# Kernel tuning notes

Hardware: AMD Instinct MI355X
Metric: run time of the kernel (lower is better)

## Reference

```python
import jax, jax.numpy as jnp
import numpy as np
import math

NUM_LAYERS_HALF = 2   # num_layers // 2
NUM_HEADS = 12
DIM = 768
FFN_DIM = 3072
VOCAB = 50257
BLOCK = 2048
LN_EPS = 1e-5


def _sinusoidal_pe(max_len, dim):
    pos = np.arange(max_len, dtype=np.float32)[:, None]
    div = np.exp(np.arange(0, dim, 2, dtype=np.float32) * (-math.log(10000.0) / dim))
    pe = np.zeros((max_len, dim), dtype=np.float32)
    pe[:, 0::2] = np.sin(pos * div)
    pe[:, 1::2] = np.cos(pos * div)
    return jnp.asarray(pe)[None]  # [1, max_len, dim]


def setup_inputs() -> dict:
    key = jax.random.key(0)
    ks = jax.random.split(key, 16)
    L, D, F = NUM_LAYERS_HALF, DIM, FFN_DIM
    s = 0.02
    return {
        "idx": jax.random.randint(ks[0], (1, 2048), 0, VOCAB),
        "token_emb": jax.random.normal(ks[1], (VOCAB, D), jnp.float32) * s,
        "pe": _sinusoidal_pe(BLOCK, D),
        "qkv_w": jax.random.normal(ks[2], (L, D, 3 * D), jnp.float32) * s,
        "qkv_b": jnp.zeros((L, 3 * D), jnp.float32),
        "out_w": jax.random.normal(ks[3], (L, D, D), jnp.float32) * s,
        "out_b": jnp.zeros((L, D), jnp.float32),
        "ln1_s": jnp.ones((L, D), jnp.float32),
        "ln1_b": jnp.zeros((L, D), jnp.float32),
        "ln2_s": jnp.ones((L, D), jnp.float32),
        "ln2_b": jnp.zeros((L, D), jnp.float32),
        "w1": jax.random.normal(ks[4], (L, D, F), jnp.float32) * s,
        "b1": jnp.zeros((L, F), jnp.float32),
        "w2": jax.random.normal(ks[5], (L, F, D), jnp.float32) * s,
        "b2": jnp.zeros((L, D), jnp.float32),
    }


def _layer_norm(x, scale, bias):
    m = jnp.mean(x, axis=-1, keepdims=True)
    v = jnp.mean(jnp.square(x - m), axis=-1, keepdims=True)
    return (x - m) * jax.lax.rsqrt(v + LN_EPS) * scale + bias


def _forward(idx, token_emb, pe, qkv_w, qkv_b, out_w, out_b,
             ln1_s, ln1_b, ln2_s, ln2_b, w1, b1, w2, b2):
    B, S = idx.shape
    D, H = DIM, NUM_HEADS
    hd = D // H
    x = token_emb[idx] + pe[:, :S]                     # [B,S,D]
    causal = jnp.tril(jnp.ones((S, S), dtype=bool))    # [S,S]

    def block(x, p):
        qw, qb, ow, ob, l1s, l1b, l2s, l2b, fw1, fb1, fw2, fb2 = p
        h = _layer_norm(x, l1s, l1b)
        qkv = (h @ qw + qb).reshape(B, S, 3, H, hd)
        q, k, v = jnp.moveaxis(qkv, 2, 0)              # each [B,S,H,hd]
        q = q.transpose(0, 2, 1, 3)                    # [B,H,S,hd]
        k = k.transpose(0, 2, 1, 3)
        v = v.transpose(0, 2, 1, 3)
        scores = jnp.einsum('bhqd,bhkd->bhqk', q, k) / math.sqrt(hd)
        scores = jnp.where(causal, scores, -1e9)
        attn = jax.nn.softmax(scores, axis=-1)
        o = jnp.einsum('bhqk,bhkd->bhqd', attn, v)
        o = o.transpose(0, 2, 1, 3).reshape(B, S, D)
        x = x + (o @ ow + ob)
        h2 = _layer_norm(x, l2s, l2b)
        ff = jax.nn.gelu(h2 @ fw1 + fb1, approximate=False) @ fw2 + fb2
        return x + ff, None

    params = (qkv_w, qkv_b, out_w, out_b, ln1_s, ln1_b, ln2_s, ln2_b, w1, b1, w2, b2)
    x, _ = jax.lax.scan(block, x, params)
    return x


def reference(idx, token_emb, pe, qkv_w, qkv_b, out_w, out_b,
              ln1_s, ln1_b, ln2_s, ln2_b, w1, b1, w2, b2):
    return _forward(idx, token_emb, pe, qkv_w, qkv_b, out_w, out_b,
                    ln1_s, ln1_b, ln2_s, ln2_b, w1, b1, w2, b2)
```

## Files before the change

kernel.cpp:

```cpp
#include <hip/hip_runtime.h>
#include <hip/hip_bf16.h>


#define SEQ 2048
#define DIM 768
#define NH 12
#define HD 64
#define FFN 3072
#define QKVD (3 * DIM)

typedef __attribute__((ext_vector_type(8))) short short8;
typedef __attribute__((ext_vector_type(4))) float f32x4;

__device__ __forceinline__ ushort bf16bits(float v) {
    __hip_bfloat16 hb = __float2bfloat16(v);
    return *reinterpret_cast<ushort*>(&hb);
}

__device__ __forceinline__ void gload_lds16(const ushort* g, ushort* l) {
    __builtin_amdgcn_global_load_lds(
        (const __attribute__((address_space(1))) void*)g,
        (__attribute__((address_space(3))) void*)l, 16, 0, 0);
}

__global__ void embed_kernel(const int* __restrict__ idx,
                             const float* __restrict__ emb,
                             const float* __restrict__ pe,
                             float* __restrict__ x) {
    int i = blockIdx.x * 256 + threadIdx.x;
    int s = i / DIM;
    int d = i - s * DIM;
    x[i] = emb[idx[s] * DIM + d] + pe[i];
}

__global__ void transpose_w(const float* __restrict__ W,
                            __hip_bfloat16* __restrict__ WT, int K, int N) {
    __shared__ float t[32][33];
    const float* Wp = W + (size_t)blockIdx.z * K * N;
    __hip_bfloat16* Tp = WT + (size_t)blockIdx.z * K * N;
    int k0 = blockIdx.y * 32, n0 = blockIdx.x * 32;
    int r = threadIdx.x >> 3, c4 = (threadIdx.x & 7) * 4;
    float4 v = *(const float4*)&Wp[(size_t)(k0 + r) * N + n0 + c4];
    t[r][c4 + 0] = v.x; t[r][c4 + 1] = v.y; t[r][c4 + 2] = v.z; t[r][c4 + 3] = v.w;
    __syncthreads();
    __hip_bfloat16* dst = &Tp[(size_t)(n0 + r) * K + k0 + c4];
#pragma unroll
    for (int j = 0; j < 4; ++j) dst[j] = __float2bfloat16(t[c4 + j][r]);
}

__global__ void ln_kernel(const float* __restrict__ x,
                          const float* __restrict__ sc,
                          const float* __restrict__ bi,
                          __hip_bfloat16* __restrict__ h) {
    int row = blockIdx.x, tid = threadIdx.x;
    __shared__ float red[256];
    const float* xr = x + row * DIM;
    float v[3];
#pragma unroll
    for (int i = 0; i < 3; ++i) v[i] = xr[tid + i * 256];
    float s = v[0] + v[1] + v[2];
    red[tid] = s; __syncthreads();
    for (int t = 128; t > 0; t >>= 1) {
        if (tid < t) red[tid] += red[tid + t];
        __syncthreads();
    }
    float mean = red[0] * (1.0f / DIM);
    __syncthreads();
    float q = 0.f;
#pragma unroll
    for (int i = 0; i < 3; ++i) { float d = v[i] - mean; q += d * d; }
    red[tid] = q; __syncthreads();
    for (int t = 128; t > 0; t >>= 1) {
        if (tid < t) red[tid] += red[tid + t];
        __syncthreads();
    }
    float rstd = rsqrtf(red[0] * (1.0f / DIM) + 1e-5f);
#pragma unroll
    for (int i = 0; i < 3; ++i) {
        int d = tid + i * 256;
        h[row * DIM + d] = __float2bfloat16((v[i] - mean) * rstd * sc[d] + bi[d]);
    }
}

template <int BN, bool GELU, bool RES, bool OUTBF16>
__global__ __launch_bounds__(256) void mfma_gemm(
        const ushort* __restrict__ A, const ushort* __restrict__ WT,
        const float* __restrict__ bias, const float* __restrict__ res,
        void* __restrict__ Cout, int M, int N, int K) {
    constexpr int NT = BN / 32;
    __shared__ ushort As[128 * 32];
    __shared__ ushort Bs[BN * 32];
    int tid = threadIdx.x;
    int w = tid >> 6, lane = tid & 63;
    int wm = (w >> 1) * 64, wn = (w & 1) * (BN / 2);
    int bm = blockIdx.y * 128, bn = blockIdx.x * BN;
    int lm = lane & 15, q8 = (lane >> 4) * 8;

    f32x4 acc[4][NT];
#pragma unroll
    for (int i = 0; i < 4; ++i)
#pragma unroll
        for (int j = 0; j < NT; ++j) acc[i][j] = {0.f, 0.f, 0.f, 0.f};

    int c0 = tid, c1 = tid + 256;
    const ushort* pa0 = &A[(size_t)(bm + (c0 >> 2)) * K + (c0 & 3) * 8];
    const ushort* pa1 = &A[(size_t)(bm + (c1 >> 2)) * K + (c1 & 3) * 8];
    const ushort* pb0 = &WT[(size_t)(bn + (c0 >> 2)) * K + (c0 & 3) * 8];
    const ushort* pb1 = nullptr;
    if constexpr (BN == 128)
        pb1 = &WT[(size_t)(bn + (c1 >> 2)) * K + (c1 & 3) * 8];

    for (int k0 = 0; k0 < K; k0 += 32) {
        __syncthreads();
        gload_lds16(pa0 + k0, &As[c0 * 8]);
        gload_lds16(pa1 + k0, &As[c1 * 8]);
        gload_lds16(pb0 + k0, &Bs[c0 * 8]);
        if constexpr (BN == 128)
            gload_lds16(pb1 + k0, &Bs[c1 * 8]);
        __syncthreads();

        short8 af[4], bw[NT];
#pragma unroll
        for (int mt = 0; mt < 4; ++mt)
            af[mt] = *(const short8*)&As[(wm + mt * 16 + lm) * 32 + q8];
#pragma unroll
        for (int nt = 0; nt < NT; ++nt)
            bw[nt] = *(const short8*)&Bs[(wn + nt * 16 + lm) * 32 + q8];
#pragma unroll
        for (int mt = 0; mt < 4; ++mt)
#pragma unroll
            for (int nt = 0; nt < NT; ++nt)
                acc[mt][nt] = __builtin_amdgcn_mfma_f32_16x16x32_bf16(
                    af[mt], bw[nt], acc[mt][nt], 0, 0, 0);
    }

#pragma unroll
    for (int nt = 0; nt < NT; ++nt) {
        int col = bn + wn + nt * 16 + lm;
        float bv = bias[col];
#pragma unroll
        for (int mt = 0; mt < 4; ++mt) {
            int rowb = bm + wm + mt * 16 + (q8 >> 1);
#pragma unroll
            for (int r = 0; r < 4; ++r) {
                int row = rowb + r;
                float v = acc[mt][nt][r] + bv;
                if (GELU) v = 0.5f * v * (1.0f + erff(v * 0.70710678118654752f));
                if (RES) v += res[(size_t)row * N + col];
                if (OUTBF16)
                    ((__hip_bfloat16*)Cout)[(size_t)row * N + col] = __float2bfloat16(v);
                else
                    ((float*)Cout)[(size_t)row * N + col] = v;
            }
        }
    }
}

__global__ __launch_bounds__(256) void flash_attn_kernel(
        const ushort* __restrict__ qkv, ushort* __restrict__ o) {
    int bi = blockIdx.x;
    int qt = 31 - bi / NH, head = bi % NH;
    int tid = threadIdx.x, w = tid >> 6, lane = tid & 63;
    int ln16 = lane & 15, quad = lane >> 4;

    __shared__ ushort Ks[2][64 * 72];
    __shared__ ushort Vt[2][64 * 64];
    __shared__ ushort Ps[4][16 * 72];

    int skey[2], sc8;
    sc8 = (tid & 7) * 8;
    skey[0] = tid >> 3;
    skey[1] = (256 + tid) >> 3;

    short8 kst[2], vst[2];
    const ushort* kbase = qkv + DIM + head * HD + sc8;

    short8 qf[2];
    {
        const ushort* qp = &qkv[(size_t)(qt * 64 + w * 16 + ln16) * QKVD
                                + head * HD + quad * 8];
        qf[0] = *(const short8*)qp;
        qf[1] = *(const short8*)(qp + 32);
    }

#pragma unroll
    for (int hh = 0; hh < 2; ++hh) {
        const ushort* kp = kbase + (size_t)(0 * 64 + skey[hh]) * QKVD;
        kst[hh] = *(const short8*)kp;
        vst[hh] = *(const short8*)(kp + DIM);
    }
#pragma unroll
    for (int hh = 0; hh < 2; ++hh) {
        int key = skey[hh];
        *(short8*)&Ks[0][key * 72 + sc8] = kst[hh];
        int g0 = key >> 3, ke = key & 7;
#pragma unroll
        for (int j = 0; j < 8; ++j) {
            int r = sc8 + j;
            Vt[0][r * 64 + ((g0 ^ (r >> 3)) & 7) * 8 + ke] = ((ushort*)&vst[hh])[j];
        }
    }
    __syncthreads();

    float m_i = -1e30f, l_i = 0.f;
    f32x4 oacc[4];
#pragma unroll
    for (int mt = 0; mt < 4; ++mt) oacc[mt] = {0.f, 0.f, 0.f, 0.f};

    int cur = 0;
    for (int kt = 0; kt <= qt; ++kt) {
        bool pre = (kt < qt);
        if (pre) {
#pragma unroll
            for (int hh = 0; hh < 2; ++hh) {
                const ushort* kp = kbase + (size_t)((kt + 1) * 64 + skey[hh]) * QKVD;
                kst[hh] = *(const short8*)kp;
                vst[hh] = *(const short8*)(kp + DIM);
            }
        }

        f32x4 s[4];
#pragma unroll
        for (int mt = 0; mt < 4; ++mt) {
            s[mt] = {0.f, 0.f, 0.f, 0.f};
#pragma unroll
            for (int kc = 0; kc < 2; ++kc) {
                short8 kf = *(const short8*)&Ks[cur][(mt * 16 + ln16) * 72
                                                     + kc * 32 + quad * 8];
                s[mt] = __builtin_amdgcn_mfma_f32_16x16x32_bf16(
                    kf, qf[kc], s[mt], 0, 0, 0);
            }
        }

        int qrow = qt * 64 + w * 16 + ln16;
        float sv[4][4];
        if (kt == qt) {
#pragma unroll
            for (int mt = 0; mt < 4; ++mt)
#pragma unroll
                for (int r = 0; r < 4; ++r) {
                    int key = kt * 64 + mt * 16 + quad * 4 + r;
                    sv[mt][r] = (key > qrow) ? -1e30f : s[mt][r] * 0.125f;
                }
        } else {
#pragma unroll
            for (int mt = 0; mt < 4; ++mt)
#pragma unroll
                for (int r = 0; r < 4; ++r) sv[mt][r] = s[mt][r] * 0.125f;
        }

        float tmax = -1e30f;
#pragma unroll
        for (int mt = 0; mt < 4; ++mt)
#pragma unroll
            for (int r = 0; r < 4; ++r) tmax = fmaxf(tmax, sv[mt][r]);
        tmax = fmaxf(tmax, __shfl_xor(tmax, 16));
        tmax = fmaxf(tmax, __shfl_xor(tmax, 32));
        float m_new = fmaxf(m_i, tmax);
        float alpha = __expf(m_i - m_new);
        m_i = m_new;

        float ls = 0.f;
#pragma unroll
        for (int mt = 0; mt < 4; ++mt) {
            union { ushort u[4]; unsigned long long ull; } pk;
#pragma unroll
            for (int r = 0; r < 4; ++r) {
                float p = __expf(sv[mt][r] - m_new);
                ls += p;
                pk.u[r] = bf16bits(p);
            }
            *(unsigned long long*)&Ps[w][ln16 * 72 + mt * 16 + quad * 4] = pk.ull;
        }
        ls += __shfl_xor(ls, 16);
        ls += __shfl_xor(ls, 32);
        l_i = l_i * alpha + ls;

#pragma unroll
        for (int mt = 0; mt < 4; ++mt) {
            oacc[mt][0] *= alpha; oacc[mt][1] *= alpha;
            oacc[mt][2] *= alpha; oacc[mt][3] *= alpha;
        }

#pragma unroll
        for (int kc = 0; kc < 2; ++kc) {
            short8 pf = *(const short8*)&Ps[w][ln16 * 72 + kc * 32 + quad * 8];
#pragma unroll
            for (int mt = 0; mt < 4; ++mt) {
                int row = mt * 16 + ln16;
                int g = kc * 4 + quad;
                short8 vf = *(const short8*)&Vt[cur][row * 64
                                                     + ((g ^ (row >> 3)) & 7) * 8];
                oacc[mt] = __builtin_amdgcn_mfma_f32_16x16x32_bf16(
                    vf, pf, oacc[mt], 0, 0, 0);
            }
        }

        if (pre) {
            int nb = cur ^ 1;
#pragma unroll
            for (int hh = 0; hh < 2; ++hh) {
                int key = skey[hh];
                *(short8*)&Ks[nb][key * 72 + sc8] = kst[hh];
                int g0 = key >> 3, ke = key & 7;
#pragma unroll
                for (int j = 0; j < 8; ++j) {
                    int r = sc8 + j;
                    Vt[nb][r * 64 + ((g0 ^ (r >> 3)) & 7) * 8 + ke] =
                        ((ushort*)&vst[hh])[j];
                }
            }
        }
        __syncthreads();
        cur ^= 1;
    }

    float inv = 1.0f / l_i;
    int orow = qt * 64 + w * 16 + ln16;
#pragma unroll
    for (int mt = 0; mt < 4; ++mt)
#pragma unroll
        for (int r = 0; r < 4; ++r) {
            int dimc = head * HD + mt * 16 + quad * 4 + r;
            o[(size_t)orow * DIM + dimc] = bf16bits(oacc[mt][r] * inv);
        }
}

extern "C" void kernel_launch(void* const* d_in, const int* in_sizes, int n_in,
                              void* d_out, int out_size, void* d_ws, size_t ws_size,
                              hipStream_t stream) {
    const int*   idx   = (const int*)  d_in[0];
    const float* emb   = (const float*)d_in[1];
    const float* pe    = (const float*)d_in[2];
    const float* qkv_w = (const float*)d_in[3];
    const float* qkv_b = (const float*)d_in[4];
    const float* out_w = (const float*)d_in[5];
    const float* out_b = (const float*)d_in[6];
    const float* ln1_s = (const float*)d_in[7];
    const float* ln1_b = (const float*)d_in[8];
    const float* ln2_s = (const float*)d_in[9];
    const float* ln2_b = (const float*)d_in[10];
    const float* w1    = (const float*)d_in[11];
    const float* b1    = (const float*)d_in[12];
    const float* w2    = (const float*)d_in[13];
    const float* b2    = (const float*)d_in[14];

    float* x = (float*)d_ws;
    __hip_bfloat16* h   = (__hip_bfloat16*)(x + SEQ * DIM);
    __hip_bfloat16* qkv = h + SEQ * DIM;
    __hip_bfloat16* ffa = qkv + (size_t)SEQ * QKVD;
    __hip_bfloat16* qkv_wT = ffa + (size_t)SEQ * FFN;
    __hip_bfloat16* out_wT = qkv_wT + (size_t)2 * QKVD * DIM;
    __hip_bfloat16* w1T    = out_wT + (size_t)2 * DIM * DIM;
    __hip_bfloat16* w2T    = w1T + (size_t)2 * FFN * DIM;

    transpose_w<<<dim3(QKVD / 32, DIM / 32, 2), 256, 0, stream>>>(qkv_w, qkv_wT, DIM, QKVD);
    transpose_w<<<dim3(DIM / 32, DIM / 32, 2), 256, 0, stream>>>(out_w, out_wT, DIM, DIM);
    transpose_w<<<dim3(FFN / 32, DIM / 32, 2), 256, 0, stream>>>(w1, w1T, DIM, FFN);
    transpose_w<<<dim3(DIM / 32, FFN / 32, 2), 256, 0, stream>>>(w2, w2T, FFN, DIM);

    embed_kernel<<<SEQ * DIM / 256, 256, 0, stream>>>(idx, emb, pe, x);

    for (int l = 0; l < 2; ++l) {
        ln_kernel<<<SEQ, 256, 0, stream>>>(x, ln1_s + l * DIM, ln1_b + l * DIM, h);
        mfma_gemm<128, false, false, true><<<dim3(QKVD / 128, SEQ / 128), 256, 0, stream>>>(
            (const ushort*)h, (const ushort*)(qkv_wT + (size_t)l * QKVD * DIM),
            qkv_b + l * QKVD, nullptr, qkv, SEQ, QKVD, DIM);
        flash_attn_kernel<<<dim3(32 * NH), 256, 0, stream>>>(
            (const ushort*)qkv, (ushort*)h);
        mfma_gemm<64, false, true, false><<<dim3(DIM / 64, SEQ / 128), 256, 0, stream>>>(
            (const ushort*)h, (const ushort*)(out_wT + (size_t)l * DIM * DIM),
            out_b + l * DIM, x, x, SEQ, DIM, DIM);
        ln_kernel<<<SEQ, 256, 0, stream>>>(x, ln2_s + l * DIM, ln2_b + l * DIM, h);
        mfma_gemm<128, true, false, true><<<dim3(FFN / 128, SEQ / 128), 256, 0, stream>>>(
            (const ushort*)h, (const ushort*)(w1T + (size_t)l * FFN * DIM),
            b1 + l * FFN, nullptr, ffa, SEQ, FFN, DIM);
        float* cdst = (l == 1) ? (float*)d_out : x;
        mfma_gemm<64, false, true, false><<<dim3(DIM / 64, SEQ / 128), 256, 0, stream>>>(
            (const ushort*)ffa, (const ushort*)(w2T + (size_t)l * DIM * FFN),
            b2 + l * DIM, x, cdst, SEQ, DIM, FFN);
    }
}
```

Baseline: 617.3 us.

## Double-buffer GEMM LDS tiles with BK=64 and XOR swizzle; merge weight transposes

The MFMA GEMM now loads 64-wide K tiles into two LDS buffers, prefetching the next tile while computing the current one, and uses one barrier per iteration instead of two. The LDS layout is XOR-swizzled by row to avoid bank conflicts on the short8 fragment reads. The four weight-transpose launches are merged into a single launch that picks its matrix from the block index. Shared memory per block roughly quadruples, which may lower occupancy.

```diff
diff --git a/kernel.cpp b/kernel.cpp
--- a/kernel.cpp
+++ b/kernel.cpp
@@ -33,12 +33,26 @@
     x[i] = emb[idx[s] * DIM + d] + pe[i];
 }
 
-__global__ void transpose_w(const float* __restrict__ W,
-                            __hip_bfloat16* __restrict__ WT, int K, int N) {
+__global__ void transpose_all(
+        const float* __restrict__ qkv_w, const float* __restrict__ out_w,
+        const float* __restrict__ w1, const float* __restrict__ w2,
+        __hip_bfloat16* __restrict__ qkv_wT, __hip_bfloat16* __restrict__ out_wT,
+        __hip_bfloat16* __restrict__ w1T, __hip_bfloat16* __restrict__ w2T) {
     __shared__ float t[32][33];
-    const float* Wp = W + (size_t)blockIdx.z * K * N;
-    __hip_bfloat16* Tp = WT + (size_t)blockIdx.z * K * N;
-    int k0 = blockIdx.y * 32, n0 = blockIdx.x * 32;
+    int b = blockIdx.x;
+    const float* W; __hip_bfloat16* T; int K, N, nx;
+    if (b < 3456)        { W = qkv_w; T = qkv_wT; K = 768;  N = 2304; nx = 72; }
+    else if (b < 4608)   { b -= 3456; W = out_w; T = out_wT; K = 768; N = 768; nx = 24; }
+    else if (b < 9216)   { b -= 4608; W = w1;    T = w1T;   K = 768;  N = 3072; nx = 96; }
+    else                 { b -= 9216; W = w2;    T = w2T;   K = 3072; N = 768;  nx = 24; }
+    int ny = K / 32;
+    int bz = b / (nx * ny);
+    int rem = b - bz * (nx * ny);
+    int by = rem / nx, bx = rem - by * nx;
+
+    const float* Wp = W + (size_t)bz * K * N;
+    __hip_bfloat16* Tp = T + (size_t)bz * K * N;
+    int k0 = by * 32, n0 = bx * 32;
     int r = threadIdx.x >> 3, c4 = (threadIdx.x & 7) * 4;
     float4 v = *(const float4*)&Wp[(size_t)(k0 + r) * N + n0 + c4];
     t[r][c4 + 0] = v.x; t[r][c4 + 1] = v.y; t[r][c4 + 2] = v.z; t[r][c4 + 3] = v.w;
@@ -88,13 +102,15 @@
         const float* __restrict__ bias, const float* __restrict__ res,
         void* __restrict__ Cout, int M, int N, int K) {
     constexpr int NT = BN / 32;
-    __shared__ ushort As[128 * 32];
-    __shared__ ushort Bs[BN * 32];
+    constexpr int NBC = BN * 8 / 256;
+    __shared__ ushort As[2][128 * 64];
+    __shared__ ushort Bs[2][BN * 64];
     int tid = threadIdx.x;
     int w = tid >> 6, lane = tid & 63;
     int wm = (w >> 1) * 64, wn = (w & 1) * (BN / 2);
     int bm = blockIdx.y * 128, bn = blockIdx.x * BN;
-    int lm = lane & 15, q8 = (lane >> 4) * 8;
+    int lm = lane & 15, quad = lane >> 4;
+    int jb = lm & 7;
 
     f32x4 acc[4][NT];
 #pragma unroll
@@ -102,38 +118,73 @@
 #pragma unroll
         for (int j = 0; j < NT; ++j) acc[i][j] = {0.f, 0.f, 0.f, 0.f};
 
-    int c0 = tid, c1 = tid + 256;
-    const ushort* pa0 = &A[(size_t)(bm + (c0 >> 2)) * K + (c0 & 3) * 8];
-    const ushort* pa1 = &A[(size_t)(bm + (c1 >> 2)) * K + (c1 & 3) * 8];
-    const ushort* pb0 = &WT[(size_t)(bn + (c0 >> 2)) * K + (c0 & 3) * 8];
-    const ushort* pb1 = nullptr;
-    if constexpr (BN == 128)
-        pb1 = &WT[(size_t)(bn + (c1 >> 2)) * K + (c1 & 3) * 8];
-
-    for (int k0 = 0; k0 < K; k0 += 32) {
+    const ushort* gA[4];
+    const ushort* gB[NBC];
+#pragma unroll
+    for (int i = 0; i < 4; ++i) {
+        int c = i * 256 + tid;
+        int row = c >> 3, j = (c & 7) ^ (row & 7);
+        gA[i] = &A[(size_t)(bm + row) * K + j * 8];
+    }
+#pragma unroll
+    for (int i = 0; i < NBC; ++i) {
+        int c = i * 256 + tid;
+        int row = c >> 3, j = (c & 7) ^ (row & 7);
+        gB[i] = &WT[(size_t)(bn + row) * K + j * 8];
+    }
+
+    const int nk = K >> 6;
+
+#pragma unroll
+    for (int i = 0; i < 4; ++i)
+        gload_lds16(gA[i], &As[0][(i * 256 + tid) * 8]);
+#pragma unroll
+    for (int i = 0; i < NBC; ++i)
+        gload_lds16(gB[i], &Bs[0][(i * 256 + tid) * 8]);
+    __syncthreads();
+
+    int p = 0;
+    for (int t = 0; t < nk; ++t) {
+        if (t + 1 < nk) {
+            int k1 = (t + 1) << 6;
+#pragma unroll
+            for (int i = 0; i < 4; ++i)
+                gload_lds16(gA[i] + k1, &As[p ^ 1][(i * 256 + tid) * 8]);
+#pragma unroll
+            for (int i = 0; i < NBC; ++i)
+                gload_lds16(gB[i] + k1, &Bs[p ^ 1][(i * 256 + tid) * 8]);
+        }
+
+        short8 af[2][4], bw[2][NT];
+#pragma unroll
+        for (int kc = 0; kc < 2; ++kc) {
+#pragma unroll
+            for (int mt = 0; mt < 4; ++mt) {
+                int row = wm + mt * 16 + lm;
+                int j = (kc * 4 + quad) ^ jb;
+                af[kc][mt] = *(const short8*)&As[p][row * 64 + j * 8];
+            }
+#pragma unroll
+            for (int nt = 0; nt < NT; ++nt) {
+                int row = wn + nt * 16 + lm;
+                int j = (kc * 4 + quad) ^ jb;
+                bw[kc][nt] = *(const short8*)&Bs[p][row * 64 + j * 8];
+            }
+        }
+#pragma unroll
+        for (int kc = 0; kc < 2; ++kc)
+#pragma unroll
+            for (int mt = 0; mt < 4; ++mt)
+#pragma unroll
+                for (int nt = 0; nt < NT; ++nt)
+                    acc[mt][nt] = __builtin_amdgcn_mfma_f32_16x16x32_bf16(
+                        af[kc][mt], bw[kc][nt], acc[mt][nt], 0, 0, 0);
+
         __syncthreads();
-        gload_lds16(pa0 + k0, &As[c0 * 8]);
-        gload_lds16(pa1 + k0, &As[c1 * 8]);
-        gload_lds16(pb0 + k0, &Bs[c0 * 8]);
-        if constexpr (BN == 128)
-            gload_lds16(pb1 + k0, &Bs[c1 * 8]);
-        __syncthreads();
-
-        short8 af[4], bw[NT];
-#pragma unroll
-        for (int mt = 0; mt < 4; ++mt)
-            af[mt] = *(const short8*)&As[(wm + mt * 16 + lm) * 32 + q8];
-#pragma unroll
-        for (int nt = 0; nt < NT; ++nt)
-            bw[nt] = *(const short8*)&Bs[(wn + nt * 16 + lm) * 32 + q8];
-#pragma unroll
-        for (int mt = 0; mt < 4; ++mt)
-#pragma unroll
-            for (int nt = 0; nt < NT; ++nt)
-                acc[mt][nt] = __builtin_amdgcn_mfma_f32_16x16x32_bf16(
-                    af[mt], bw[nt], acc[mt][nt], 0, 0, 0);
-    }
-
+        p ^= 1;
+    }
+
+    int q8 = quad * 8;
 #pragma unroll
     for (int nt = 0; nt < NT; ++nt) {
         int col = bn + wn + nt * 16 + lm;
@@ -354,10 +405,8 @@
     __hip_bfloat16* w1T    = out_wT + (size_t)2 * DIM * DIM;
     __hip_bfloat16* w2T    = w1T + (size_t)2 * FFN * DIM;
 
-    transpose_w<<<dim3(QKVD / 32, DIM / 32, 2), 256, 0, stream>>>(qkv_w, qkv_wT, DIM, QKVD);
-    transpose_w<<<dim3(DIM / 32, DIM / 32, 2), 256, 0, stream>>>(out_w, out_wT, DIM, DIM);
-    transpose_w<<<dim3(FFN / 32, DIM / 32, 2), 256, 0, stream>>>(w1, w1T, DIM, FFN);
-    transpose_w<<<dim3(DIM / 32, FFN / 32, 2), 256, 0, stream>>>(w2, w2T, FFN, DIM);
+    transpose_all<<<13824, 256, 0, stream>>>(qkv_w, out_w, w1, w2,
+                                             qkv_wT, out_wT, w1T, w2T);
 
     embed_kernel<<<SEQ * DIM / 256, 256, 0, stream>>>(idx, emb, pe, x);
 
```

After: 566.0 us. 8.3% less time.
